# Kernel optimization log

Measured on AMD Instinct MI355X. Metric: run time of the kernel, lower is better.

Reference implementation:

```python
import jax, jax.numpy as jnp
import numpy as np

N_NODES = 50000
N_EDGES = 1600000
NODE_DIM = 64
HIDDEN_DIM = 128
EDGE_DIM = 32


def _linear_params(key, fan_in, fan_out, bias=True):
    k1, k2 = jax.random.split(key)
    bound = 1.0 / np.sqrt(fan_in)
    W = jax.random.uniform(k1, (fan_in, fan_out), minval=-bound, maxval=bound, dtype=jnp.float32)
    if bias:
        b = jax.random.uniform(k2, (fan_out,), minval=-bound, maxval=bound, dtype=jnp.float32)
        return W, b
    return W, None


def setup_inputs() -> dict:
    key = jax.random.key(0)
    ks = jax.random.split(key, 12)
    h = jax.random.normal(ks[0], (N_NODES, NODE_DIM), dtype=jnp.float32)
    x = jax.random.normal(ks[1], (N_NODES, 3), dtype=jnp.float32) * 10.0
    edge_index = jax.random.randint(ks[2], (2, N_EDGES), 0, N_NODES, dtype=jnp.int32).astype(jnp.int64)
    edge_dist = jax.random.uniform(ks[3], (N_EDGES,), dtype=jnp.float32) * 10.0

    msg_in = 2 * NODE_DIM + EDGE_DIM
    node_w1, node_b1 = _linear_params(ks[4], msg_in, HIDDEN_DIM)
    node_w2, node_b2 = _linear_params(ks[5], HIDDEN_DIM, NODE_DIM)
    coord_w1, coord_b1 = _linear_params(ks[6], msg_in, HIDDEN_DIM)
    coord_w2, _ = _linear_params(ks[7], HIDDEN_DIM, 1, bias=False)
    edge_w1, edge_b1 = _linear_params(ks[8], 1, EDGE_DIM)
    edge_w2, edge_b2 = _linear_params(ks[9], EDGE_DIM, EDGE_DIM)

    return dict(h=h, x=x, edge_index=edge_index, edge_dist=edge_dist,
                node_w1=node_w1, node_b1=node_b1, node_w2=node_w2, node_b2=node_b2,
                coord_w1=coord_w1, coord_b1=coord_b1, coord_w2=coord_w2,
                edge_w1=edge_w1, edge_b1=edge_b1, edge_w2=edge_w2, edge_b2=edge_b2)


def reference(h, x, edge_index, edge_dist,
              node_w1, node_b1, node_w2, node_b2,
              coord_w1, coord_b1, coord_w2,
              edge_w1, edge_b1, edge_w2, edge_b2):
    src = edge_index[0]
    dst = edge_index[1]

    # edge_mlp: Linear(1, edge_dim) -> SiLU -> Linear(edge_dim, edge_dim)
    edge_attr = jax.nn.silu(edge_dist[:, None] @ edge_w1 + edge_b1) @ edge_w2 + edge_b2

    # per-edge message input: [E, 2*node_dim + edge_dim]
    m_input = jnp.concatenate([h[src], h[dst], edge_attr], axis=-1)

    # node_mlp: Linear -> SiLU -> Linear
    m = jax.nn.silu(m_input @ node_w1 + node_b1) @ node_w2 + node_b2
    h_agg = jnp.zeros_like(h).at[dst].add(m)

    # coord_mlp: Linear -> SiLU -> Linear(hidden, 1, bias=False)
    coord_weight = jax.nn.silu(m_input @ coord_w1 + coord_b1) @ coord_w2  # [E, 1]

    dir_vec = x[src] - x[dst]                               # [E, 3]
    dir_len = jnp.maximum(jnp.linalg.norm(dir_vec, axis=-1, keepdims=True), 1e-8)
    coord_update = coord_weight * (dir_vec / dir_len)
    x_agg = jnp.zeros_like(x).at[dst].add(coord_update)

    return (h + h_agg, x + x_agg)
```

## Files before the change

### kernel.cpp

```cpp
#include <hip/hip_runtime.h>
#include <hip/hip_bf16.h>
#include <stdint.h>

#define NN 50000
#define NE 1600000
#define BE 128

typedef __attribute__((ext_vector_type(8))) short short8;
typedef __attribute__((ext_vector_type(4))) float f32x4;

__device__ __forceinline__ unsigned short f2bf(float f) {
    unsigned int u = __float_as_uint(f);
    u += 0x7fff + ((u >> 16) & 1);
    return (unsigned short)(u >> 16);
}

__device__ __forceinline__ unsigned int pk2bf(float lo, float hi) {
    __hip_bfloat162 b = __float22bfloat162_rn(float2{lo, hi});
    return *(unsigned int*)&b;
}

__device__ __forceinline__ float silu_f(float v) {
    return v * __builtin_amdgcn_rcpf(1.0f + __expf(-v));
}

#define WS_EW2T_US   49152
#define WS_HB_B      100352
#define WS_XP_B      6500352
#define WS_HB_NEED   6500352
#define WS_XP_NEED   7300352

__global__ void prep_kernel(const float* __restrict__ nw1,
                            const float* __restrict__ cw1,
                            const float* __restrict__ nw2,
                            const float* __restrict__ ew2,
                            unsigned short* __restrict__ ws) {
    int i = blockIdx.x * 256 + threadIdx.x;
    if (i < 20480) {
        int n = i / 160, k = i % 160;
        ws[i] = f2bf(nw1[k * 128 + n]);
    } else if (i < 40960) {
        int j = i - 20480; int n = j / 160, k = j % 160;
        ws[i] = f2bf(cw1[k * 128 + n]);
    } else if (i < 49152) {
        int j = i - 40960; int o = j / 128, k = j % 128;
        ws[i] = f2bf(nw2[k * 64 + o]);
    } else if (i < 50176) {
        int j = i - 49152; int jo = j >> 5, k = j & 31;
        ws[i] = f2bf(ew2[k * 32 + jo]);
    }
}

__global__ void hcvt_kernel(const float4* __restrict__ h4,
                            unsigned short* __restrict__ hb) {
    int i = blockIdx.x * 256 + threadIdx.x;
    if (i < 800000) {
        float4 v = h4[i];
        uint2 u;
        u.x = pk2bf(v.x, v.y);
        u.y = pk2bf(v.z, v.w);
        *(uint2*)&hb[i * 4] = u;
    }
}

__global__ void xpack_kernel(const float* __restrict__ x,
                             float4* __restrict__ xp) {
    int n = blockIdx.x * 256 + threadIdx.x;
    if (n < NN) {
        xp[n] = float4{x[n * 3], x[n * 3 + 1], x[n * 3 + 2], 0.f};
    }
}

__global__ void init_out(const float4* __restrict__ h4,
                         const float4* __restrict__ x4,
                         float4* __restrict__ out4) {
    int i = blockIdx.x * 256 + threadIdx.x;
    if (i < 800000)       out4[i] = h4[i];
    else if (i < 837500)  out4[i] = x4[i - 800000];
}

#define MIS 168

__global__ __launch_bounds__(256, 3)
void egnn_edge_kernel(const float* __restrict__ h,
                      const unsigned short* __restrict__ hb,
                      const float* __restrict__ x,
                      const float4* __restrict__ xp,
                      const int* __restrict__ eidx,
                      const float* __restrict__ edist,
                      const float* __restrict__ node_b1,
                      const float* __restrict__ node_b2,
                      const float* __restrict__ coord_b1,
                      const float* __restrict__ coord_w2,
                      const float* __restrict__ ew1,
                      const float* __restrict__ eb1,
                      const float* __restrict__ eb2,
                      const unsigned short* __restrict__ ws,
                      float* __restrict__ out_h,
                      float* __restrict__ out_x) {
    __shared__ unsigned short mi[BE * MIS];
    __shared__ int srcS[BE];
    __shared__ int dstS[BE];

    const int tid  = threadIdx.x;
    const int w    = tid >> 6;
    const int lane = tid & 63;
    const int ln   = lane & 15;
    const int quad = lane >> 4;
    const int e0   = blockIdx.x * BE;

    if (tid < BE)      srcS[tid]       = eidx[e0 + tid];
    else               dstS[tid - BE]  = eidx[NE + e0 + tid - BE];
    __syncthreads();

    if (hb) {
        const uint2* hb2 = (const uint2*)hb;
        const int g = tid >> 4, l16 = tid & 15;
        #pragma unroll
        for (int it = 0; it < 16; ++it) {
            int row = it * 16 + g;
            int e = row & 127;
            int node = (row < 128) ? srcS[e] : dstS[e];
            int cbase = (row < 128) ? 0 : 64;
            *(uint2*)&mi[e * MIS + cbase + l16 * 4] = hb2[node * 16 + l16];
        }
    } else {
        const float4* h4 = (const float4*)h;
        const int g = tid >> 4, l16 = tid & 15;
        #pragma unroll
        for (int it = 0; it < 16; ++it) {
            int row = it * 16 + g;
            int e = row & 127;
            int node = (row < 128) ? srcS[e] : dstS[e];
            int cbase = (row < 128) ? 0 : 64;
            float4 v = h4[node * 16 + l16];
            uint2 u;
            u.x = pk2bf(v.x, v.y);
            u.y = pk2bf(v.z, v.w);
            *(uint2*)&mi[e * MIS + cbase + l16 * 4] = u;
        }
    }
    {
        int e = tid >> 1, half = tid & 1;
        float d = edist[e0 + e];
        float t[16];
        #pragma unroll
        for (int j = 0; j < 16; ++j) {
            int k = half * 16 + j;
            t[j] = silu_f(d * ew1[k] + eb1[k]);
        }
        uint4 u0, u1;
        u0.x = pk2bf(t[0], t[1]);   u0.y = pk2bf(t[2], t[3]);
        u0.z = pk2bf(t[4], t[5]);   u0.w = pk2bf(t[6], t[7]);
        u1.x = pk2bf(t[8], t[9]);   u1.y = pk2bf(t[10], t[11]);
        u1.z = pk2bf(t[12], t[13]); u1.w = pk2bf(t[14], t[15]);
        *(uint4*)&mi[e * MIS + 128 + half * 16]     = u0;
        *(uint4*)&mi[e * MIS + 128 + half * 16 + 8] = u1;
    }

    __syncthreads();

    const int arow0 = (w * 32 + ln) * MIS;
    const int arow1 = (w * 32 + 16 + ln) * MIS;
    const int koff  = quad * 8;
    const f32x4 zero = {0.f, 0.f, 0.f, 0.f};

    {
        const unsigned short* e2T = ws + WS_EW2T_US;
        short8 ta0 = *(const short8*)&mi[arow0 + 128 + koff];
        short8 ta1 = *(const short8*)&mi[arow1 + 128 + koff];
        f32x4 ea[2][2];
        ea[0][0] = zero; ea[0][1] = zero; ea[1][0] = zero; ea[1][1] = zero;
        #pragma unroll
        for (int nt = 0; nt < 2; ++nt) {
            short8 b = *(const short8*)(e2T + (nt * 16 + ln) * 32 + koff);
            ea[0][nt] = __builtin_amdgcn_mfma_f32_16x16x32_bf16(ta0, b, ea[0][nt], 0, 0, 0);
            ea[1][nt] = __builtin_amdgcn_mfma_f32_16x16x32_bf16(ta1, b, ea[1][nt], 0, 0, 0);
        }
        #pragma unroll
        for (int nt = 0; nt < 2; ++nt) {
            int col = nt * 16 + ln;
            float bv = eb2[col];
            #pragma unroll
            for (int rt = 0; rt < 2; ++rt) {
                #pragma unroll
                for (int r = 0; r < 4; ++r)
                    mi[(w * 32 + rt * 16 + quad * 4 + r) * MIS + 128 + col] =
                        f2bf(ea[rt][nt][r] + bv);
            }
        }
    }

    short8 aA[5], aB[5];
    #pragma unroll
    for (int kc = 0; kc < 5; ++kc) {
        aA[kc] = *(const short8*)&mi[arow0 + kc * 32 + koff];
        aB[kc] = *(const short8*)&mi[arow1 + kc * 32 + koff];
    }

    const int wvoff = ln * 160 + koff;

    f32x4 accC[2][8];
    #pragma unroll
    for (int a = 0; a < 2; ++a)
        #pragma unroll
        for (int b = 0; b < 8; ++b) accC[a][b] = zero;
    {
        const unsigned short* wsrc = ws + 20480;
        #pragma unroll
        for (int half = 0; half < 2; ++half) {
            #pragma unroll
            for (int kc = 0; kc < 5; ++kc) {
                #pragma unroll
                for (int nt = 0; nt < 4; ++nt) {
                    short8 b = *(const short8*)(wsrc + half * 10240 + nt * 2560
                                                + kc * 32 + wvoff);
                    const int nn = half * 4 + nt;
                    accC[0][nn] = __builtin_amdgcn_mfma_f32_16x16x32_bf16(aA[kc], b, accC[0][nn], 0, 0, 0);
                    accC[1][nn] = __builtin_amdgcn_mfma_f32_16x16x32_bf16(aB[kc], b, accC[1][nn], 0, 0, 0);
                }
            }
        }
    }

    {
        float cw[2][4];
        #pragma unroll
        for (int mt = 0; mt < 2; ++mt)
            #pragma unroll
            for (int r = 0; r < 4; ++r) cw[mt][r] = 0.f;
        #pragma unroll
        for (int nt = 0; nt < 8; ++nt) {
            int col = nt * 16 + ln;
            float b1v = coord_b1[col];
            float w2v = coord_w2[col];
            #pragma unroll
            for (int mt = 0; mt < 2; ++mt)
                #pragma unroll
                for (int r = 0; r < 4; ++r)
                    cw[mt][r] += silu_f(accC[mt][nt][r] + b1v) * w2v;
        }
        #pragma unroll
        for (int off = 1; off < 16; off <<= 1) {
            #pragma unroll
            for (int mt = 0; mt < 2; ++mt)
                #pragma unroll
                for (int r = 0; r < 4; ++r)
                    cw[mt][r] += __shfl_xor(cw[mt][r], off, 64);
        }
        if (ln < 8) {
            const int smt = ln >> 2, sr = ln & 3;
            float cwsel = 0.f;
            #pragma unroll
            for (int mt = 0; mt < 2; ++mt)
                #pragma unroll
                for (int r = 0; r < 4; ++r)
                    cwsel = (mt == smt && r == sr) ? cw[mt][r] : cwsel;
            int lrow = w * 32 + smt * 16 + quad * 4 + sr;
            int s = srcS[lrow], dn = dstS[lrow];
            float dx, dy, dz;
            if (xp) {
                float4 xs = xp[s], xd = xp[dn];
                dx = xs.x - xd.x; dy = xs.y - xd.y; dz = xs.z - xd.z;
            } else {
                dx = x[s * 3]     - x[dn * 3];
                dy = x[s * 3 + 1] - x[dn * 3 + 1];
                dz = x[s * 3 + 2] - x[dn * 3 + 2];
            }
            float len = fmaxf(sqrtf(dx * dx + dy * dy + dz * dz), 1e-8f);
            float k = cwsel * __builtin_amdgcn_rcpf(len);
            atomicAdd(out_x + dn * 3,     k * dx);
            atomicAdd(out_x + dn * 3 + 1, k * dy);
            atomicAdd(out_x + dn * 3 + 2, k * dz);
        }
    }

    f32x4 accN[2][8];
    #pragma unroll
    for (int a = 0; a < 2; ++a)
        #pragma unroll
        for (int b = 0; b < 8; ++b) accN[a][b] = zero;
    {
        const unsigned short* wsrc = ws;
        #pragma unroll
        for (int half = 0; half < 2; ++half) {
            #pragma unroll
            for (int kc = 0; kc < 5; ++kc) {
                #pragma unroll
                for (int nt = 0; nt < 4; ++nt) {
                    short8 b = *(const short8*)(wsrc + half * 10240 + nt * 2560
                                                + kc * 32 + wvoff);
                    const int nn = half * 4 + nt;
                    accN[0][nn] = __builtin_amdgcn_mfma_f32_16x16x32_bf16(aA[kc], b, accN[0][nn], 0, 0, 0);
                    accN[1][nn] = __builtin_amdgcn_mfma_f32_16x16x32_bf16(aB[kc], b, accN[1][nn], 0, 0, 0);
                }
            }
        }
    }

    #pragma unroll
    for (int mt = 0; mt < 2; ++mt) {
        const int rowb = (w * 32 + mt * 16 + quad * 4) * MIS;
        #pragma unroll
        for (int nt = 0; nt < 8; ++nt) {
            int col = nt * 16 + ln;
            float b1v = node_b1[col];
            #pragma unroll
            for (int r = 0; r < 4; ++r)
                mi[rowb + r * MIS + col] = f2bf(silu_f(accN[mt][nt][r] + b1v));
        }
    }

    f32x4 acc2[2][4];
    #pragma unroll
    for (int a = 0; a < 2; ++a)
        #pragma unroll
        for (int b = 0; b < 4; ++b) acc2[a][b] = zero;
    const unsigned short* nw2T = ws + 40960;
    #pragma unroll
    for (int kc = 0; kc < 4; ++kc) {
        short8 a0 = *(const short8*)&mi[arow0 + kc * 32 + koff];
        short8 a1 = *(const short8*)&mi[arow1 + kc * 32 + koff];
        #pragma unroll
        for (int nt = 0; nt < 4; ++nt) {
            short8 b = *(const short8*)(nw2T + (nt * 16 + ln) * 128 + kc * 32 + koff);
            acc2[0][nt] = __builtin_amdgcn_mfma_f32_16x16x32_bf16(a0, b, acc2[0][nt], 0, 0, 0);
            acc2[1][nt] = __builtin_amdgcn_mfma_f32_16x16x32_bf16(a1, b, acc2[1][nt], 0, 0, 0);
        }
    }
    #pragma unroll
    for (int mt = 0; mt < 2; ++mt) {
        #pragma unroll
        for (int r = 0; r < 4; ++r) {
            int lrow = w * 32 + mt * 16 + quad * 4 + r;
            int dn = dstS[lrow];
            float* outrow = out_h + (size_t)dn * 64;
            #pragma unroll
            for (int nt = 0; nt < 4; ++nt) {
                int col = nt * 16 + ln;
                atomicAdd(outrow + col, acc2[mt][nt][r] + node_b2[col]);
            }
        }
    }
}

extern "C" void kernel_launch(void* const* d_in, const int* in_sizes, int n_in,
                              void* d_out, int out_size, void* d_ws, size_t ws_size,
                              hipStream_t stream) {
    const float* h    = (const float*)d_in[0];
    const float* x    = (const float*)d_in[1];
    const int*   eidx = (const int*)d_in[2];
    const float* edist= (const float*)d_in[3];
    const float* nw1  = (const float*)d_in[4];
    const float* nb1  = (const float*)d_in[5];
    const float* nw2  = (const float*)d_in[6];
    const float* nb2  = (const float*)d_in[7];
    const float* cw1  = (const float*)d_in[8];
    const float* cb1  = (const float*)d_in[9];
    const float* cw2  = (const float*)d_in[10];
    const float* ew1  = (const float*)d_in[11];
    const float* eb1  = (const float*)d_in[12];
    const float* ew2  = (const float*)d_in[13];
    const float* eb2  = (const float*)d_in[14];
    float* out = (float*)d_out;
    unsigned short* ws = (unsigned short*)d_ws;

    prep_kernel<<<196, 256, 0, stream>>>(nw1, cw1, nw2, ew2, ws);
    init_out<<<3272, 256, 0, stream>>>((const float4*)h, (const float4*)x, (float4*)out);

    unsigned short* hb = nullptr;
    float4* xp = nullptr;
    if (ws_size >= (size_t)WS_HB_NEED) {
        hb = (unsigned short*)((char*)d_ws + WS_HB_B);
        hcvt_kernel<<<3125, 256, 0, stream>>>((const float4*)h, hb);
    }
    if (ws_size >= (size_t)WS_XP_NEED) {
        xp = (float4*)((char*)d_ws + WS_XP_B);
        xpack_kernel<<<196, 256, 0, stream>>>(x, xp);
    }

    egnn_edge_kernel<<<NE / BE, 256, 0, stream>>>(h, hb, x, xp, eidx, edist,
                                                  nb1, nb2, cb1, cw2,
                                                  ew1, eb1, eb2,
                                                  ws, out, out + 3200000);
}
```

Before: 742.3 us.

## Use single-wave blocks per 32 edges and fuse init kernels

The edge kernel moves from 256-thread blocks covering 128 edges to 64-thread single-wavefront blocks covering 32 edges. Edge indices now stay in registers and are shared with __shfl, which removes the shared srcS/dstS arrays and every __syncthreads. The separate h-convert, x-pack and output-init kernels are merged into one fused_init launch to cut launch overhead. In exchange the kernel launches many more small blocks, and each block reloads the weight B-operands from global memory for only 32 edges, which lowers weight reuse per fetch.

```diff
diff --git a/kernel.cpp b/kernel.cpp
--- a/kernel.cpp
+++ b/kernel.cpp
@@ -4,7 +4,7 @@
 
 #define NN 50000
 #define NE 1600000
-#define BE 128
+#define BE 32
 
 typedef __attribute__((ext_vector_type(8))) short short8;
 typedef __attribute__((ext_vector_type(4))) float f32x4;
@@ -51,37 +51,34 @@
     }
 }
 
-__global__ void hcvt_kernel(const float4* __restrict__ h4,
-                            unsigned short* __restrict__ hb) {
+__global__ void fused_init(const float4* __restrict__ h4,
+                           const float* __restrict__ x,
+                           const float4* __restrict__ x4,
+                           float4* __restrict__ out4,
+                           unsigned short* __restrict__ hb,
+                           float4* __restrict__ xp) {
     int i = blockIdx.x * 256 + threadIdx.x;
     if (i < 800000) {
         float4 v = h4[i];
-        uint2 u;
-        u.x = pk2bf(v.x, v.y);
-        u.y = pk2bf(v.z, v.w);
-        *(uint2*)&hb[i * 4] = u;
-    }
-}
-
-__global__ void xpack_kernel(const float* __restrict__ x,
-                             float4* __restrict__ xp) {
-    int n = blockIdx.x * 256 + threadIdx.x;
-    if (n < NN) {
-        xp[n] = float4{x[n * 3], x[n * 3 + 1], x[n * 3 + 2], 0.f};
-    }
-}
-
-__global__ void init_out(const float4* __restrict__ h4,
-                         const float4* __restrict__ x4,
-                         float4* __restrict__ out4) {
-    int i = blockIdx.x * 256 + threadIdx.x;
-    if (i < 800000)       out4[i] = h4[i];
-    else if (i < 837500)  out4[i] = x4[i - 800000];
+        out4[i] = v;
+        if (hb) {
+            uint2 u;
+            u.x = pk2bf(v.x, v.y);
+            u.y = pk2bf(v.z, v.w);
+            *(uint2*)&hb[i * 4] = u;
+        }
+    } else if (i < 850000) {
+        int n = i - 800000;
+        if (xp) xp[n] = float4{x[n * 3], x[n * 3 + 1], x[n * 3 + 2], 0.f};
+    } else if (i < 887500) {
+        int j = i - 850000;
+        out4[800000 + j] = x4[j];
+    }
 }
 
 #define MIS 168
 
-__global__ __launch_bounds__(256, 3)
+__global__ __launch_bounds__(64, 4)
 void egnn_edge_kernel(const float* __restrict__ h,
                       const unsigned short* __restrict__ hb,
                       const float* __restrict__ x,
@@ -99,50 +96,19 @@
                       float* __restrict__ out_h,
                       float* __restrict__ out_x) {
     __shared__ unsigned short mi[BE * MIS];
-    __shared__ int srcS[BE];
-    __shared__ int dstS[BE];
-
-    const int tid  = threadIdx.x;
-    const int w    = tid >> 6;
-    const int lane = tid & 63;
-    const int ln   = lane & 15;
-    const int quad = lane >> 4;
+
+    const int l    = threadIdx.x;
+    const int ln   = l & 15;
+    const int quad = l >> 4;
     const int e0   = blockIdx.x * BE;
 
-    if (tid < BE)      srcS[tid]       = eidx[e0 + tid];
-    else               dstS[tid - BE]  = eidx[NE + e0 + tid - BE];
-    __syncthreads();
-
-    if (hb) {
-        const uint2* hb2 = (const uint2*)hb;
-        const int g = tid >> 4, l16 = tid & 15;
-        #pragma unroll
-        for (int it = 0; it < 16; ++it) {
-            int row = it * 16 + g;
-            int e = row & 127;
-            int node = (row < 128) ? srcS[e] : dstS[e];
-            int cbase = (row < 128) ? 0 : 64;
-            *(uint2*)&mi[e * MIS + cbase + l16 * 4] = hb2[node * 16 + l16];
-        }
-    } else {
-        const float4* h4 = (const float4*)h;
-        const int g = tid >> 4, l16 = tid & 15;
-        #pragma unroll
-        for (int it = 0; it < 16; ++it) {
-            int row = it * 16 + g;
-            int e = row & 127;
-            int node = (row < 128) ? srcS[e] : dstS[e];
-            int cbase = (row < 128) ? 0 : 64;
-            float4 v = h4[node * 16 + l16];
-            uint2 u;
-            u.x = pk2bf(v.x, v.y);
-            u.y = pk2bf(v.z, v.w);
-            *(uint2*)&mi[e * MIS + cbase + l16 * 4] = u;
-        }
-    }
-    {
-        int e = tid >> 1, half = tid & 1;
-        float d = edist[e0 + e];
+    const int me   = l & 31;
+    const int msrc = eidx[e0 + me];
+    const int mdst = eidx[NE + e0 + me];
+
+    {
+        const int e = l >> 1, half = l & 1;
+        const float d = edist[e0 + e];
         float t[16];
         #pragma unroll
         for (int j = 0; j < 16; ++j) {
@@ -158,10 +124,33 @@
         *(uint4*)&mi[e * MIS + 128 + half * 16 + 8] = u1;
     }
 
-    __syncthreads();
-
-    const int arow0 = (w * 32 + ln) * MIS;
-    const int arow1 = (w * 32 + 16 + ln) * MIS;
+    if (hb) {
+        const uint2* hb2 = (const uint2*)hb;
+        #pragma unroll
+        for (int it = 0; it < 16; ++it) {
+            const int e = ((it & 7) << 2) + quad;
+            const int node = (it < 8) ? __shfl(msrc, e, 64) : __shfl(mdst, e, 64);
+            const int cbase = (it < 8) ? 0 : 64;
+            *(uint2*)&mi[e * MIS + cbase + ln * 4] = hb2[node * 16 + ln];
+        }
+    } else {
+        const float4* h4 = (const float4*)h;
+        #pragma unroll
+        for (int it = 0; it < 16; ++it) {
+            const int e = ((it & 7) << 2) + quad;
+            const int node = (it < 8) ? __shfl(msrc, e, 64) : __shfl(mdst, e, 64);
+            const int cbase = (it < 8) ? 0 : 64;
+            float4 v = h4[node * 16 + ln];
+            uint2 u;
+            u.x = pk2bf(v.x, v.y);
+            u.y = pk2bf(v.z, v.w);
+            *(uint2*)&mi[e * MIS + cbase + ln * 4] = u;
+        }
+    }
+
+
+    const int arow0 = ln * MIS;
+    const int arow1 = (16 + ln) * MIS;
     const int koff  = quad * 8;
     const f32x4 zero = {0.f, 0.f, 0.f, 0.f};
 
@@ -185,7 +174,7 @@
             for (int rt = 0; rt < 2; ++rt) {
                 #pragma unroll
                 for (int r = 0; r < 4; ++r)
-                    mi[(w * 32 + rt * 16 + quad * 4 + r) * MIS + 128 + col] =
+                    mi[(rt * 16 + quad * 4 + r) * MIS + 128 + col] =
                         f2bf(ea[rt][nt][r] + bv);
             }
         }
@@ -248,16 +237,17 @@
                 for (int r = 0; r < 4; ++r)
                     cw[mt][r] += __shfl_xor(cw[mt][r], off, 64);
         }
+        const int smt = (ln >> 2) & 1, sr = ln & 3;
+        const int lrow = (smt * 16 + quad * 4 + sr) & 31;
+        const int s  = __shfl(msrc, lrow, 64);
+        const int dn = __shfl(mdst, lrow, 64);
         if (ln < 8) {
-            const int smt = ln >> 2, sr = ln & 3;
             float cwsel = 0.f;
             #pragma unroll
             for (int mt = 0; mt < 2; ++mt)
                 #pragma unroll
                 for (int r = 0; r < 4; ++r)
                     cwsel = (mt == smt && r == sr) ? cw[mt][r] : cwsel;
-            int lrow = w * 32 + smt * 16 + quad * 4 + sr;
-            int s = srcS[lrow], dn = dstS[lrow];
             float dx, dy, dz;
             if (xp) {
                 float4 xs = xp[s], xd = xp[dn];
@@ -300,7 +290,7 @@
 
     #pragma unroll
     for (int mt = 0; mt < 2; ++mt) {
-        const int rowb = (w * 32 + mt * 16 + quad * 4) * MIS;
+        const int rowb = (mt * 16 + quad * 4) * MIS;
         #pragma unroll
         for (int nt = 0; nt < 8; ++nt) {
             int col = nt * 16 + ln;
@@ -332,8 +322,8 @@
     for (int mt = 0; mt < 2; ++mt) {
         #pragma unroll
         for (int r = 0; r < 4; ++r) {
-            int lrow = w * 32 + mt * 16 + quad * 4 + r;
-            int dn = dstS[lrow];
+            int lrow = mt * 16 + quad * 4 + r;
+            int dn = __shfl(mdst, lrow, 64);
             float* outrow = out_h + (size_t)dn * 64;
             #pragma unroll
             for (int nt = 0; nt < 4; ++nt) {
@@ -365,22 +355,17 @@
     float* out = (float*)d_out;
     unsigned short* ws = (unsigned short*)d_ws;
 
-    prep_kernel<<<196, 256, 0, stream>>>(nw1, cw1, nw2, ew2, ws);
-    init_out<<<3272, 256, 0, stream>>>((const float4*)h, (const float4*)x, (float4*)out);
-
     unsigned short* hb = nullptr;
     float4* xp = nullptr;
-    if (ws_size >= (size_t)WS_HB_NEED) {
-        hb = (unsigned short*)((char*)d_ws + WS_HB_B);
-        hcvt_kernel<<<3125, 256, 0, stream>>>((const float4*)h, hb);
-    }
-    if (ws_size >= (size_t)WS_XP_NEED) {
-        xp = (float4*)((char*)d_ws + WS_XP_B);
-        xpack_kernel<<<196, 256, 0, stream>>>(x, xp);
-    }
-
-    egnn_edge_kernel<<<NE / BE, 256, 0, stream>>>(h, hb, x, xp, eidx, edist,
-                                                  nb1, nb2, cb1, cw2,
-                                                  ew1, eb1, eb2,
-                                                  ws, out, out + 3200000);
-}
+    if (ws_size >= (size_t)WS_HB_NEED) hb = (unsigned short*)((char*)d_ws + WS_HB_B);
+    if (ws_size >= (size_t)WS_XP_NEED) xp = (float4*)((char*)d_ws + WS_XP_B);
+
+    prep_kernel<<<196, 256, 0, stream>>>(nw1, cw1, nw2, ew2, ws);
+    fused_init<<<3468, 256, 0, stream>>>((const float4*)h, x, (const float4*)x,
+                                         (float4*)out, hb, xp);
+
+    egnn_edge_kernel<<<NE / BE, 64, 0, stream>>>(h, hb, x, xp, eidx, edist,
+                                                 nb1, nb2, cb1, cw2,
+                                                 ew1, eb1, eb2,
+                                                 ws, out, out + 3200000);
+}
```

After: 798.9 us. 1.08x slower.

## Sort edges by destination and aggregate segments before atomic scatter

Applied to the files above, without the earlier changes.

Adds a counting sort of edges by destination (histogram, single-block scan, atomic scatter) and a new edge kernel that reads the sorted edges. It reduces consecutive rows sharing a destination before issuing atomics, which is meant to cut global atomic traffic to the node outputs and improve locality on dst gathers. It also fuses the output init, bf16 conversion and x packing into one kernel. The cost is extra sort passes, a serial single-block scan, and a workspace need of about 26.7 MB. Without that workspace it falls back to the old kernel.

```diff
diff --git a/kernel.cpp b/kernel.cpp
--- a/kernel.cpp
+++ b/kernel.cpp
@@ -29,6 +29,11 @@
 #define WS_XP_B      6500352
 #define WS_HB_NEED   6500352
 #define WS_XP_NEED   7300352
+#define WS_HIST_B    7300352
+#define WS_SRC_B     7501056
+#define WS_DST_B     13901056
+#define WS_DIST_B    20301056
+#define WS_SORT_NEED 26701056
 
 __global__ void prep_kernel(const float* __restrict__ nw1,
                             const float* __restrict__ cw1,
@@ -51,35 +56,383 @@
     }
 }
 
-__global__ void hcvt_kernel(const float4* __restrict__ h4,
-                            unsigned short* __restrict__ hb) {
+__global__ void fused_init(const float4* __restrict__ h4,
+                           const float* __restrict__ x,
+                           const float4* __restrict__ x4,
+                           float4* __restrict__ out4,
+                           unsigned short* __restrict__ hb,
+                           float4* __restrict__ xp) {
     int i = blockIdx.x * 256 + threadIdx.x;
     if (i < 800000) {
         float4 v = h4[i];
-        uint2 u;
-        u.x = pk2bf(v.x, v.y);
-        u.y = pk2bf(v.z, v.w);
-        *(uint2*)&hb[i * 4] = u;
-    }
-}
-
-__global__ void xpack_kernel(const float* __restrict__ x,
-                             float4* __restrict__ xp) {
-    int n = blockIdx.x * 256 + threadIdx.x;
-    if (n < NN) {
-        xp[n] = float4{x[n * 3], x[n * 3 + 1], x[n * 3 + 2], 0.f};
-    }
-}
-
-__global__ void init_out(const float4* __restrict__ h4,
-                         const float4* __restrict__ x4,
-                         float4* __restrict__ out4) {
+        out4[i] = v;
+        if (hb) {
+            uint2 u;
+            u.x = pk2bf(v.x, v.y);
+            u.y = pk2bf(v.z, v.w);
+            *(uint2*)&hb[i * 4] = u;
+        }
+    } else if (i < 850000) {
+        int n = i - 800000;
+        if (xp) xp[n] = float4{x[n * 3], x[n * 3 + 1], x[n * 3 + 2], 0.f};
+    } else if (i < 887500) {
+        int j = i - 850000;
+        out4[800000 + j] = x4[j];
+    }
+}
+
+__global__ void zero_hist(int* __restrict__ hist) {
     int i = blockIdx.x * 256 + threadIdx.x;
-    if (i < 800000)       out4[i] = h4[i];
-    else if (i < 837500)  out4[i] = x4[i - 800000];
+    if (i < NN) hist[i] = 0;
+}
+
+__global__ void hist_kernel(const int* __restrict__ eidx, int* __restrict__ hist) {
+    int e = blockIdx.x * 256 + threadIdx.x;
+    if (e < NE) atomicAdd(&hist[eidx[NE + e]], 1);
+}
+
+__global__ __launch_bounds__(1024)
+void scan_kernel(int* __restrict__ hist) {
+    __shared__ int tmp[1024];
+    __shared__ int carry;
+    const int tid = threadIdx.x;
+    if (tid == 0) carry = 0;
+    __syncthreads();
+    for (int base = 0; base < NN; base += 1024) {
+        int v = (base + tid < NN) ? hist[base + tid] : 0;
+        tmp[tid] = v;
+        __syncthreads();
+        #pragma unroll
+        for (int off = 1; off < 1024; off <<= 1) {
+            int t = (tid >= off) ? tmp[tid - off] : 0;
+            __syncthreads();
+            tmp[tid] += t;
+            __syncthreads();
+        }
+        int excl = carry + tmp[tid] - v;
+        if (base + tid < NN) hist[base + tid] = excl;
+        __syncthreads();
+        if (tid == 1023) carry += tmp[1023];
+        __syncthreads();
+    }
+}
+
+__global__ void scatter_kernel(const int* __restrict__ eidx,
+                               const float* __restrict__ edist,
+                               int* __restrict__ offs,
+                               int* __restrict__ src_s,
+                               int* __restrict__ dst_s,
+                               float* __restrict__ dist_s) {
+    int e = blockIdx.x * 256 + threadIdx.x;
+    if (e < NE) {
+        int d = eidx[NE + e];
+        int p = atomicAdd(&offs[d], 1);
+        src_s[p]  = eidx[e];
+        dst_s[p]  = d;
+        dist_s[p] = edist[e];
+    }
 }
 
 #define MIS 168
+#define MAS 84
+
+__global__ __launch_bounds__(256, 3)
+void egnn_edge_sorted(const float* __restrict__ h,
+                      const unsigned short* __restrict__ hb,
+                      const float* __restrict__ x,
+                      const float4* __restrict__ xp,
+                      const int* __restrict__ src_s,
+                      const int* __restrict__ dst_s,
+                      const float* __restrict__ dist_s,
+                      const float* __restrict__ node_b1,
+                      const float* __restrict__ node_b2,
+                      const float* __restrict__ coord_b1,
+                      const float* __restrict__ coord_w2,
+                      const float* __restrict__ ew1,
+                      const float* __restrict__ eb1,
+                      const float* __restrict__ eb2,
+                      const unsigned short* __restrict__ ws,
+                      float* __restrict__ out_h,
+                      float* __restrict__ out_x) {
+    __shared__ unsigned short mi[BE * MIS];
+    __shared__ int srcS[BE];
+    __shared__ int dstS[BE];
+    __shared__ float xacc[BE][3];
+
+    const int tid  = threadIdx.x;
+    const int w    = tid >> 6;
+    const int lane = tid & 63;
+    const int ln   = lane & 15;
+    const int quad = lane >> 4;
+    const int e0   = blockIdx.x * BE;
+
+    if (tid < BE)      srcS[tid]      = src_s[e0 + tid];
+    else               dstS[tid - BE] = dst_s[e0 + tid - BE];
+    __syncthreads();
+
+    if (hb) {
+        const uint2* hb2 = (const uint2*)hb;
+        const int g = tid >> 4, l16 = tid & 15;
+        #pragma unroll
+        for (int it = 0; it < 16; ++it) {
+            int row = it * 16 + g;
+            int e = row & 127;
+            int node = (row < 128) ? srcS[e] : dstS[e];
+            int cbase = (row < 128) ? 0 : 64;
+            *(uint2*)&mi[e * MIS + cbase + l16 * 4] = hb2[node * 16 + l16];
+        }
+    } else {
+        const float4* h4 = (const float4*)h;
+        const int g = tid >> 4, l16 = tid & 15;
+        #pragma unroll
+        for (int it = 0; it < 16; ++it) {
+            int row = it * 16 + g;
+            int e = row & 127;
+            int node = (row < 128) ? srcS[e] : dstS[e];
+            int cbase = (row < 128) ? 0 : 64;
+            float4 v = h4[node * 16 + l16];
+            uint2 u;
+            u.x = pk2bf(v.x, v.y);
+            u.y = pk2bf(v.z, v.w);
+            *(uint2*)&mi[e * MIS + cbase + l16 * 4] = u;
+        }
+    }
+    {
+        int e = tid >> 1, half = tid & 1;
+        float d = dist_s[e0 + e];
+        float t[16];
+        #pragma unroll
+        for (int j = 0; j < 16; ++j) {
+            int k = half * 16 + j;
+            t[j] = silu_f(d * ew1[k] + eb1[k]);
+        }
+        uint4 u0, u1;
+        u0.x = pk2bf(t[0], t[1]);   u0.y = pk2bf(t[2], t[3]);
+        u0.z = pk2bf(t[4], t[5]);   u0.w = pk2bf(t[6], t[7]);
+        u1.x = pk2bf(t[8], t[9]);   u1.y = pk2bf(t[10], t[11]);
+        u1.z = pk2bf(t[12], t[13]); u1.w = pk2bf(t[14], t[15]);
+        *(uint4*)&mi[e * MIS + 128 + half * 16]     = u0;
+        *(uint4*)&mi[e * MIS + 128 + half * 16 + 8] = u1;
+    }
+
+    __syncthreads();
+
+    const int arow0 = (w * 32 + ln) * MIS;
+    const int arow1 = (w * 32 + 16 + ln) * MIS;
+    const int koff  = quad * 8;
+    const f32x4 zero = {0.f, 0.f, 0.f, 0.f};
+
+    {
+        const unsigned short* e2T = ws + WS_EW2T_US;
+        short8 ta0 = *(const short8*)&mi[arow0 + 128 + koff];
+        short8 ta1 = *(const short8*)&mi[arow1 + 128 + koff];
+        f32x4 ea[2][2];
+        ea[0][0] = zero; ea[0][1] = zero; ea[1][0] = zero; ea[1][1] = zero;
+        #pragma unroll
+        for (int nt = 0; nt < 2; ++nt) {
+            short8 b = *(const short8*)(e2T + (nt * 16 + ln) * 32 + koff);
+            ea[0][nt] = __builtin_amdgcn_mfma_f32_16x16x32_bf16(ta0, b, ea[0][nt], 0, 0, 0);
+            ea[1][nt] = __builtin_amdgcn_mfma_f32_16x16x32_bf16(ta1, b, ea[1][nt], 0, 0, 0);
+        }
+        #pragma unroll
+        for (int nt = 0; nt < 2; ++nt) {
+            int col = nt * 16 + ln;
+            float bv = eb2[col];
+            #pragma unroll
+            for (int rt = 0; rt < 2; ++rt) {
+                #pragma unroll
+                for (int r = 0; r < 4; ++r)
+                    mi[(w * 32 + rt * 16 + quad * 4 + r) * MIS + 128 + col] =
+                        f2bf(ea[rt][nt][r] + bv);
+            }
+        }
+    }
+
+    short8 aA[5], aB[5];
+    #pragma unroll
+    for (int kc = 0; kc < 5; ++kc) {
+        aA[kc] = *(const short8*)&mi[arow0 + kc * 32 + koff];
+        aB[kc] = *(const short8*)&mi[arow1 + kc * 32 + koff];
+    }
+
+    const int wvoff = ln * 160 + koff;
+
+    f32x4 accC[2][8];
+    #pragma unroll
+    for (int a = 0; a < 2; ++a)
+        #pragma unroll
+        for (int b = 0; b < 8; ++b) accC[a][b] = zero;
+    {
+        const unsigned short* wsrc = ws + 20480;
+        #pragma unroll
+        for (int half = 0; half < 2; ++half) {
+            #pragma unroll
+            for (int kc = 0; kc < 5; ++kc) {
+                #pragma unroll
+                for (int nt = 0; nt < 4; ++nt) {
+                    short8 b = *(const short8*)(wsrc + half * 10240 + nt * 2560
+                                                + kc * 32 + wvoff);
+                    const int nn = half * 4 + nt;
+                    accC[0][nn] = __builtin_amdgcn_mfma_f32_16x16x32_bf16(aA[kc], b, accC[0][nn], 0, 0, 0);
+                    accC[1][nn] = __builtin_amdgcn_mfma_f32_16x16x32_bf16(aB[kc], b, accC[1][nn], 0, 0, 0);
+                }
+            }
+        }
+    }
+
+    {
+        float cw[2][4];
+        #pragma unroll
+        for (int mt = 0; mt < 2; ++mt)
+            #pragma unroll
+            for (int r = 0; r < 4; ++r) cw[mt][r] = 0.f;
+        #pragma unroll
+        for (int nt = 0; nt < 8; ++nt) {
+            int col = nt * 16 + ln;
+            float b1v = coord_b1[col];
+            float w2v = coord_w2[col];
+            #pragma unroll
+            for (int mt = 0; mt < 2; ++mt)
+                #pragma unroll
+                for (int r = 0; r < 4; ++r)
+                    cw[mt][r] += silu_f(accC[mt][nt][r] + b1v) * w2v;
+        }
+        #pragma unroll
+        for (int off = 1; off < 16; off <<= 1) {
+            #pragma unroll
+            for (int mt = 0; mt < 2; ++mt)
+                #pragma unroll
+                for (int r = 0; r < 4; ++r)
+                    cw[mt][r] += __shfl_xor(cw[mt][r], off, 64);
+        }
+        if (ln < 8) {
+            const int smt = ln >> 2, sr = ln & 3;
+            float cwsel = 0.f;
+            #pragma unroll
+            for (int mt = 0; mt < 2; ++mt)
+                #pragma unroll
+                for (int r = 0; r < 4; ++r)
+                    cwsel = (mt == smt && r == sr) ? cw[mt][r] : cwsel;
+            int lrow = w * 32 + smt * 16 + quad * 4 + sr;
+            int s = srcS[lrow], dn = dstS[lrow];
+            float dx, dy, dz;
+            if (xp) {
+                float4 xs = xp[s], xd = xp[dn];
+                dx = xs.x - xd.x; dy = xs.y - xd.y; dz = xs.z - xd.z;
+            } else {
+                dx = x[s * 3]     - x[dn * 3];
+                dy = x[s * 3 + 1] - x[dn * 3 + 1];
+                dz = x[s * 3 + 2] - x[dn * 3 + 2];
+            }
+            float len = fmaxf(sqrtf(dx * dx + dy * dy + dz * dz), 1e-8f);
+            float k = cwsel * __builtin_amdgcn_rcpf(len);
+            xacc[lrow][0] = k * dx;
+            xacc[lrow][1] = k * dy;
+            xacc[lrow][2] = k * dz;
+        }
+    }
+
+    f32x4 accN[2][8];
+    #pragma unroll
+    for (int a = 0; a < 2; ++a)
+        #pragma unroll
+        for (int b = 0; b < 8; ++b) accN[a][b] = zero;
+    {
+        const unsigned short* wsrc = ws;
+        #pragma unroll
+        for (int half = 0; half < 2; ++half) {
+            #pragma unroll
+            for (int kc = 0; kc < 5; ++kc) {
+                #pragma unroll
+                for (int nt = 0; nt < 4; ++nt) {
+                    short8 b = *(const short8*)(wsrc + half * 10240 + nt * 2560
+                                                + kc * 32 + wvoff);
+                    const int nn = half * 4 + nt;
+                    accN[0][nn] = __builtin_amdgcn_mfma_f32_16x16x32_bf16(aA[kc], b, accN[0][nn], 0, 0, 0);
+                    accN[1][nn] = __builtin_amdgcn_mfma_f32_16x16x32_bf16(aB[kc], b, accN[1][nn], 0, 0, 0);
+                }
+            }
+        }
+    }
+
+    #pragma unroll
+    for (int mt = 0; mt < 2; ++mt) {
+        const int rowb = (w * 32 + mt * 16 + quad * 4) * MIS;
+        #pragma unroll
+        for (int nt = 0; nt < 8; ++nt) {
+            int col = nt * 16 + ln;
+            float b1v = node_b1[col];
+            #pragma unroll
+            for (int r = 0; r < 4; ++r)
+                mi[rowb + r * MIS + col] = f2bf(silu_f(accN[mt][nt][r] + b1v));
+        }
+    }
+
+    f32x4 acc2[2][4];
+    #pragma unroll
+    for (int a = 0; a < 2; ++a)
+        #pragma unroll
+        for (int b = 0; b < 4; ++b) acc2[a][b] = zero;
+    const unsigned short* nw2T = ws + 40960;
+    #pragma unroll
+    for (int kc = 0; kc < 4; ++kc) {
+        short8 a0 = *(const short8*)&mi[arow0 + kc * 32 + koff];
+        short8 a1 = *(const short8*)&mi[arow1 + kc * 32 + koff];
+        #pragma unroll
+        for (int nt = 0; nt < 4; ++nt) {
+            short8 b = *(const short8*)(nw2T + (nt * 16 + ln) * 128 + kc * 32 + koff);
+            acc2[0][nt] = __builtin_amdgcn_mfma_f32_16x16x32_bf16(a0, b, acc2[0][nt], 0, 0, 0);
+            acc2[1][nt] = __builtin_amdgcn_mfma_f32_16x16x32_bf16(a1, b, acc2[1][nt], 0, 0, 0);
+        }
+    }
+
+    __syncthreads();
+    float* macc = (float*)mi;
+    #pragma unroll
+    for (int mt = 0; mt < 2; ++mt) {
+        #pragma unroll
+        for (int r = 0; r < 4; ++r) {
+            int lrow = w * 32 + mt * 16 + quad * 4 + r;
+            #pragma unroll
+            for (int nt = 0; nt < 4; ++nt) {
+                int col = nt * 16 + ln;
+                macc[lrow * MAS + col] = acc2[mt][nt][r] + node_b2[col];
+            }
+        }
+    }
+    __syncthreads();
+
+    {
+        const int col = tid & 63;
+        const int q   = tid >> 6;
+        const int r0  = q * 32;
+        float sum = 0.f;
+        int prev = dstS[r0];
+        for (int r = r0; r < r0 + 32; ++r) {
+            int d = dstS[r];
+            if (d != prev) {
+                atomicAdd(out_h + (size_t)prev * 64 + col, sum);
+                sum = 0.f; prev = d;
+            }
+            sum += macc[r * MAS + col];
+        }
+        atomicAdd(out_h + (size_t)prev * 64 + col, sum);
+
+        if (col < 3) {
+            float xs = 0.f;
+            int pv = dstS[r0];
+            for (int r = r0; r < r0 + 32; ++r) {
+                int d = dstS[r];
+                if (d != pv) {
+                    atomicAdd(out_x + pv * 3 + col, xs);
+                    xs = 0.f; pv = d;
+                }
+                xs += xacc[r][col];
+            }
+            atomicAdd(out_x + pv * 3 + col, xs);
+        }
+    }
+}
 
 __global__ __launch_bounds__(256, 3)
 void egnn_edge_kernel(const float* __restrict__ h,
@@ -365,22 +718,34 @@
     float* out = (float*)d_out;
     unsigned short* ws = (unsigned short*)d_ws;
 
-    prep_kernel<<<196, 256, 0, stream>>>(nw1, cw1, nw2, ew2, ws);
-    init_out<<<3272, 256, 0, stream>>>((const float4*)h, (const float4*)x, (float4*)out);
-
     unsigned short* hb = nullptr;
     float4* xp = nullptr;
-    if (ws_size >= (size_t)WS_HB_NEED) {
-        hb = (unsigned short*)((char*)d_ws + WS_HB_B);
-        hcvt_kernel<<<3125, 256, 0, stream>>>((const float4*)h, hb);
-    }
-    if (ws_size >= (size_t)WS_XP_NEED) {
-        xp = (float4*)((char*)d_ws + WS_XP_B);
-        xpack_kernel<<<196, 256, 0, stream>>>(x, xp);
-    }
-
-    egnn_edge_kernel<<<NE / BE, 256, 0, stream>>>(h, hb, x, xp, eidx, edist,
-                                                  nb1, nb2, cb1, cw2,
-                                                  ew1, eb1, eb2,
-                                                  ws, out, out + 3200000);
-}
+    if (ws_size >= (size_t)WS_HB_NEED) hb = (unsigned short*)((char*)d_ws + WS_HB_B);
+    if (ws_size >= (size_t)WS_XP_NEED) xp = (float4*)((char*)d_ws + WS_XP_B);
+
+    prep_kernel<<<196, 256, 0, stream>>>(nw1, cw1, nw2, ew2, ws);
+    fused_init<<<3468, 256, 0, stream>>>((const float4*)h, x, (const float4*)x,
+                                         (float4*)out, hb, xp);
+
+    if (ws_size >= (size_t)WS_SORT_NEED) {
+        int*   hist   = (int*)((char*)d_ws + WS_HIST_B);
+        int*   src_s  = (int*)((char*)d_ws + WS_SRC_B);
+        int*   dst_s  = (int*)((char*)d_ws + WS_DST_B);
+        float* dist_s = (float*)((char*)d_ws + WS_DIST_B);
+        zero_hist<<<196, 256, 0, stream>>>(hist);
+        hist_kernel<<<NE / 256, 256, 0, stream>>>(eidx, hist);
+        scan_kernel<<<1, 1024, 0, stream>>>(hist);
+        scatter_kernel<<<NE / 256, 256, 0, stream>>>(eidx, edist, hist,
+                                                     src_s, dst_s, dist_s);
+        egnn_edge_sorted<<<NE / BE, 256, 0, stream>>>(h, hb, x, xp,
+                                                      src_s, dst_s, dist_s,
+                                                      nb1, nb2, cb1, cw2,
+                                                      ew1, eb1, eb2,
+                                                      ws, out, out + 3200000);
+    } else {
+        egnn_edge_kernel<<<NE / BE, 256, 0, stream>>>(h, hb, x, xp, eidx, edist,
+                                                      nb1, nb2, cb1, cw2,
+                                                      ew1, eb1, eb2,
+                                                      ws, out, out + 3200000);
+    }
+}
```

Result: slower. 807.1 us (+8.7%).
